# Kernel tuning notes

Hardware: AMD Instinct MI355X
Metric: run time of the kernel (lower is better)

The kernel has to match this reference:

```python
import jax, jax.numpy as jnp
import numpy as np

T = 512        # sequence / max_length
I = 512        # input_dim
H = 1024       # hidden_size
O = 1          # output_size
L = 512        # max_length (attention logits)


def setup_inputs() -> dict:
    key = jax.random.key(0)
    ks = jax.random.split(key, 14)
    s = 0.02
    return {
        "input_seq": jax.random.normal(ks[0], (T, I), jnp.float32),
        "target_seq": jax.random.normal(ks[1], (T, O), jnp.float32),
        # encoder LSTM (input I -> hidden H), PyTorch gate order i,f,g,o
        "W_ih_e": jax.random.normal(ks[2], (4 * H, I), jnp.float32) * s,
        "W_hh_e": jax.random.normal(ks[3], (4 * H, H), jnp.float32) * s,
        "b_ih_e": jnp.zeros((4 * H,), jnp.float32),
        "b_hh_e": jnp.zeros((4 * H,), jnp.float32),
        # attention: Linear(2H -> L)
        "W_attn": jax.random.normal(ks[4], (L, 2 * H), jnp.float32) * s,
        "b_attn": jnp.zeros((L,), jnp.float32),
        # decoder LSTM (input 2H -> hidden H)
        "W_ih_d": jax.random.normal(ks[5], (4 * H, 2 * H), jnp.float32) * s,
        "W_hh_d": jax.random.normal(ks[6], (4 * H, H), jnp.float32) * s,
        "b_ih_d": jnp.zeros((4 * H,), jnp.float32),
        "b_hh_d": jnp.zeros((4 * H,), jnp.float32),
        # output Linear(H -> O)
        "W_out": jax.random.normal(ks[7], (O, H), jnp.float32) * s,
        "b_out": jnp.zeros((O,), jnp.float32),
    }


def _lstm_cell(x, h, c, Wih, Whh, bih, bhh):
    gates = Wih @ x + bih + Whh @ h + bhh          # [4H]
    i, f, g, o = jnp.split(gates, 4)
    c = jax.nn.sigmoid(f) * c + jax.nn.sigmoid(i) * jnp.tanh(g)
    h = jax.nn.sigmoid(o) * jnp.tanh(c)
    return h, c


def reference(input_seq, target_seq, W_ih_e, W_hh_e, b_ih_e, b_hh_e,
              W_attn, b_attn, W_ih_d, W_hh_d, b_ih_d, b_hh_d, W_out, b_out):
    Th = input_seq.shape[0]
    max_len = W_attn.shape[0]
    hid = W_hh_e.shape[1]

    def step(carry, xs):
        eh, ec, dh, dc, aw = carry
        x_t, i = xs
        eh, ec = _lstm_cell(x_t, eh, ec, W_ih_e, W_hh_e, b_ih_e, b_hh_e)
        energy = W_attn @ jnp.concatenate([eh, dh]) + b_attn   # [L]
        aw = aw.at[i].set(energy[i])
        aw = jax.nn.softmax(aw)                                 # re-softmaxed each step, as in source
        context = aw[i] * eh                                    # [H]
        din = jnp.concatenate([context, dh])                    # [2H]
        dh, dc = _lstm_cell(din, dh, dc, W_ih_d, W_hh_d, b_ih_d, b_hh_d)
        out_t = W_out @ dh + b_out                              # [O]
        return (eh, ec, dh, dc, aw), out_t

    z = jnp.zeros((hid,), input_seq.dtype)
    carry0 = (z, z, z, z, jnp.zeros((max_len,), input_seq.dtype))
    _, output_seq = jax.lax.scan(step, carry0, (input_seq, jnp.arange(Th)))
    return output_seq  # [T, O]
```

## Files before the change

kernel.cpp:

```cpp
#include <hip/hip_runtime.h>
#include <math.h>


#define T_STEPS 512
#define ENC_BLK 128
#define NBLK    256
#define SPIN_LIMIT 200000u

typedef float fv4 __attribute__((ext_vector_type(4)));

__device__ __forceinline__ float sigf(float x) { return 1.0f / (1.0f + expf(-x)); }

__device__ __forceinline__ unsigned ld_u(unsigned* p) {
  return __hip_atomic_load(p, __ATOMIC_RELAXED, __HIP_MEMORY_SCOPE_AGENT);
}
__device__ __forceinline__ void st_u(unsigned* p, unsigned v) {
  __hip_atomic_store(p, v, __ATOMIC_RELAXED, __HIP_MEMORY_SCOPE_AGENT);
}

__device__ __forceinline__ fv4 ld_bypass16(const float* p) {
  fv4 v;
  asm volatile("global_load_dwordx4 %0, %1, off sc0 sc1\n\t"
               "s_waitcnt vmcnt(0)"
               : "=&v"(v) : "v"(p) : "memory");
  return v;
}
__device__ __forceinline__ void st_bypass16(float* p, fv4 v) {
  asm volatile("global_store_dwordx4 %0, %1, off sc0 sc1"
               :: "v"(p), "v"(v) : "memory");
}

__device__ __forceinline__ bool valid4(fv4 v) {
  return __float_as_uint(v.x) != 0xAAAAAAAAu && __float_as_uint(v.y) != 0xAAAAAAAAu &&
         __float_as_uint(v.z) != 0xAAAAAAAAu && __float_as_uint(v.w) != 0xAAAAAAAAu;
}

__device__ __forceinline__ fv4 poll_data(const float* p, unsigned* abortf, int* okp) {
  fv4 v;
  unsigned spins = 0;
  int ok = 1;
  for (;;) {
    v = ld_bypass16(p);
    if (valid4(v)) break;
    if (((++spins) & 63u) == 0u) {
      if (ld_u(abortf) != 0u || spins > SPIN_LIMIT) { ok = 0; break; }
    }
  }
  *okp = ok;
  return v;
}

__global__ __launch_bounds__(256) void prep_gemm(const float* __restrict__ X,
                                                 const float* __restrict__ Wih,
                                                 const float* __restrict__ bih,
                                                 const float* __restrict__ bhh,
                                                 float* __restrict__ px,
                                                 unsigned* abortf) {
  if (blockIdx.x == 0 && blockIdx.y == 0 && threadIdx.x == 0) st_u(abortf, 0u);
  __shared__ float Ws[64][68];
  __shared__ float Xs[64][68];
  const int r0 = blockIdx.x * 64;
  const int t0 = blockIdx.y * 64;
  const int tid = threadIdx.x;
  const int tr = tid & 15;
  const int tc = tid >> 4;
  float acc[4][4] = {{0.f}};
  for (int k0 = 0; k0 < 512; k0 += 64) {
    __syncthreads();
    const int lr = tid >> 4;
    const int lc = (tid & 15) * 4;
#pragma unroll
    for (int rep = 0; rep < 4; rep++) {
      const int row = lr + rep * 16;
      const float4 wv = *(const float4*)&Wih[(size_t)(r0 + row) * 512 + k0 + lc];
      Ws[lc + 0][row] = wv.x; Ws[lc + 1][row] = wv.y;
      Ws[lc + 2][row] = wv.z; Ws[lc + 3][row] = wv.w;
      const float4 xv = *(const float4*)&X[(size_t)(t0 + row) * 512 + k0 + lc];
      Xs[row][lc + 0] = xv.x; Xs[row][lc + 1] = xv.y;
      Xs[row][lc + 2] = xv.z; Xs[row][lc + 3] = xv.w;
    }
    __syncthreads();
    for (int kk = 0; kk < 64; kk++) {
      float a[4], x[4];
#pragma unroll
      for (int i = 0; i < 4; i++) a[i] = Ws[kk][tr * 4 + i];
#pragma unroll
      for (int j = 0; j < 4; j++) x[j] = Xs[tc * 4 + j][kk];
#pragma unroll
      for (int i = 0; i < 4; i++)
#pragma unroll
        for (int j = 0; j < 4; j++) acc[i][j] += a[i] * x[j];
    }
  }
#pragma unroll
  for (int i = 0; i < 4; i++) {
    const int r = r0 + tr * 4 + i;
    const int g = r >> 10, h = r & 1023;
    const float bsum = bih[r] + bhh[r];
#pragma unroll
    for (int j = 0; j < 4; j++) {
      const int t = t0 + tc * 4 + j;
      px[((size_t)t * 1024 + h) * 4 + g] = acc[i][j] + bsum;
    }
  }
}

__global__ __launch_bounds__(256, 1) void lstm_persist(
    const float* __restrict__ Whhe, const float* __restrict__ Wattn,
    const float* __restrict__ battn, const float* __restrict__ Wihd,
    const float* __restrict__ Whhd, const float* __restrict__ bihd,
    const float* __restrict__ bhhd, const float* __restrict__ Wout,
    const float* __restrict__ bout, const float* __restrict__ px,
    float* ehbuf, float* dhbuf, unsigned* abortf, float* out) {
  __shared__ float4 xbuf[256];
  __shared__ float4 dbuf[256];
  __shared__ float  aw[512];
  __shared__ float  GA[32];
  __shared__ float  GB[32];
  __shared__ float  redE[4];
  __shared__ float  redE2[4];
  __shared__ float  red[8];
  __shared__ float  red2[4];
  __shared__ float  bd[32];
  __shared__ int    sbad;

  const int b    = blockIdx.x;
  const int tid  = threadIdx.x;
  const int w    = tid >> 6;
  const int lane = tid & 63;
  const int jj   = lane & 7;
  const int seg  = lane >> 3;

  if (b < ENC_BLK) {
    const int e = b;
    const int r = (w << 10) + (e << 3) + jj;
    float4 we[32];
#pragma unroll
    for (int k = 0; k < 32; k++) {
      const int m = (k + seg) & 31;
      we[k] = *(const float4*)&Whhe[(size_t)r * 1024 + seg * 128 + m * 4];
    }
    xbuf[tid] = make_float4(0.f, 0.f, 0.f, 0.f);
    if (tid == 0) sbad = 0;
    float ec = 0.f;
    __syncthreads();

    for (int t = 0; t < T_STEPS; t++) {
      float pxv = 0.f;
      if (seg == 0) pxv = px[((size_t)t * 1024 + (e << 3) + jj) * 4 + w];
      float ge = 0.f;
#pragma unroll
      for (int k = 0; k < 32; k++) {
        const int m = (k + seg) & 31;
        const float4 x = xbuf[seg * 32 + m];
        ge += we[k].x * x.x + we[k].y * x.y + we[k].z * x.z + we[k].w * x.w;
      }
      ge += __shfl_xor(ge, 8, 64);
      ge += __shfl_xor(ge, 16, 64);
      ge += __shfl_xor(ge, 32, 64);
      if (seg == 0) GA[(w << 3) + jj] = ge + pxv;
      __syncthreads();
      float h = 0.f;
      if (tid < 8) {
        const float gi = GA[tid], gf = GA[8 + tid], gg = GA[16 + tid], go = GA[24 + tid];
        const float c = sigf(gf) * ec + sigf(gi) * tanhf(gg);
        ec = c;
        h = sigf(go) * tanhf(c);
      }
      if (w == 0) {
        const int base = lane & 4;
        fv4 pk;
        pk.x = __shfl(h, base + 0, 64); pk.y = __shfl(h, base + 1, 64);
        pk.z = __shfl(h, base + 2, 64); pk.w = __shfl(h, base + 3, 64);
        if (lane == 0 || lane == 4)
          st_bypass16(&ehbuf[(size_t)t * 1024 + (e << 3) + base], pk);
      }
      int ok;
      const fv4 ev = poll_data(&ehbuf[(size_t)t * 1024 + tid * 4], abortf, &ok);
      if (!ok) { st_u(abortf, 1u); sbad = 1; }
      xbuf[tid] = make_float4(ev.x, ev.y, ev.z, ev.w);
      __syncthreads();
      if (sbad) break;
    }
  } else {
    const int d = b - ENC_BLK;
    const int r = (w << 10) + (d << 3) + jj;
    float4 w1[32], wr[32];
#pragma unroll
    for (int k = 0; k < 32; k++) {
      const int m = (k + seg) & 31;
      w1[k] = *(const float4*)&Wihd[(size_t)r * 2048 + seg * 128 + m * 4];
      const float4 a = *(const float4*)&Wihd[(size_t)r * 2048 + 1024 + seg * 128 + m * 4];
      const float4 c = *(const float4*)&Whhd[(size_t)r * 1024 + seg * 128 + m * 4];
      wr[k] = make_float4(a.x + c.x, a.y + c.y, a.z + c.z, a.w + c.w);
    }
    if (tid < 32) {
      const int g = tid >> 3, j = tid & 7;
      bd[tid] = bihd[(g << 10) + (d << 3) + j] + bhhd[(g << 10) + (d << 3) + j];
    }
    xbuf[tid] = make_float4(0.f, 0.f, 0.f, 0.f);
    dbuf[tid] = make_float4(0.f, 0.f, 0.f, 0.f);
    aw[tid] = 0.f; aw[tid + 256] = 0.f;
    if (tid == 0) sbad = 0;
    float dc = 0.f;
    const float4 wo = *(const float4*)&Wout[tid * 4];
    const float boutv = bout[0];
    __syncthreads();

    bool failed = false;
    for (int t = 0; t < T_STEPS; t++) {
      const float4 wae = *(const float4*)&Wattn[(size_t)t * 2048 + tid * 4];
      const float4 wad = *(const float4*)&Wattn[(size_t)t * 2048 + 1024 + tid * 4];
      const float battn_t = battn[t];
      const float ex0 = expf(aw[tid]);
      const float ex1 = expf(aw[tid + 256]);
      float so = ((tid == t) ? 0.f : ex0) + ((tid + 256 == t) ? 0.f : ex1);
#pragma unroll
      for (int mk = 1; mk <= 32; mk <<= 1) so += __shfl_xor(so, mk, 64);
      if (lane == 0) red[w] = so;

      int ok1;
      const fv4 ev = poll_data(&ehbuf[(size_t)t * 1024 + tid * 4], abortf, &ok1);
      if (!ok1) { st_u(abortf, 1u); sbad = 1; }
      float epe = wae.x * ev.x + wae.y * ev.y + wae.z * ev.z + wae.w * ev.w;
#pragma unroll
      for (int mk = 1; mk <= 32; mk <<= 1) epe += __shfl_xor(epe, mk, 64);
      if (lane == 0) redE[w] = epe;
      xbuf[tid] = make_float4(ev.x, ev.y, ev.z, ev.w);
      __syncthreads();
      if (sbad) { failed = true; break; }

      float g1 = 0.f;
#pragma unroll
      for (int k = 0; k < 32; k++) {
        const int m = (k + seg) & 31;
        const float4 x = xbuf[seg * 32 + m];
        g1 += w1[k].x * x.x + w1[k].y * x.y + w1[k].z * x.z + w1[k].w * x.w;
      }
      g1 += __shfl_xor(g1, 8, 64); g1 += __shfl_xor(g1, 16, 64); g1 += __shfl_xor(g1, 32, 64);
      if (seg == 0) GA[(w << 3) + jj] = g1;

      fv4 dv = {0.f, 0.f, 0.f, 0.f};
      float epd = 0.f;
      if (t > 0) {
        int ok2;
        dv = poll_data(&dhbuf[(size_t)(t - 1) * 1024 + tid * 4], abortf, &ok2);
        if (!ok2) { st_u(abortf, 1u); sbad = 1; }
        epd = wad.x * dv.x + wad.y * dv.y + wad.z * dv.z + wad.w * dv.w;
      }
#pragma unroll
      for (int mk = 1; mk <= 32; mk <<= 1) epd += __shfl_xor(epd, mk, 64);
      if (lane == 0) redE2[w] = epd;
      dbuf[tid] = make_float4(dv.x, dv.y, dv.z, dv.w);
      __syncthreads();
      if (sbad) { failed = true; break; }

      float g2 = 0.f;
#pragma unroll
      for (int k = 0; k < 32; k++) {
        const int m = (k + seg) & 31;
        const float4 dd = dbuf[seg * 32 + m];
        g2 += wr[k].x * dd.x + wr[k].y * dd.y + wr[k].z * dd.z + wr[k].w * dd.w;
      }
      g2 += __shfl_xor(g2, 8, 64); g2 += __shfl_xor(g2, 16, 64); g2 += __shfl_xor(g2, 32, 64);
      if (seg == 0) GB[(w << 3) + jj] = g2;

      const float sum_other = red[0] + red[1] + red[2] + red[3];
      const float e_t = redE[0] + redE[1] + redE[2] + redE[3] +
                        redE2[0] + redE2[1] + redE2[2] + redE2[3] + battn_t;
      const float exden = expf(e_t);
      const float inv = 1.f / (sum_other + exden);
      aw[tid] = ((tid == t) ? exden : ex0) * inv;
      aw[tid + 256] = ((tid + 256 == t) ? exden : ex1) * inv;
      const float awt = exden * inv;
      __syncthreads();

      float h = 0.f;
      if (tid < 8) {
        const float gi = awt * GA[tid]      + GB[tid]      + bd[tid];
        const float gf = awt * GA[8 + tid]  + GB[8 + tid]  + bd[8 + tid];
        const float gg = awt * GA[16 + tid] + GB[16 + tid] + bd[16 + tid];
        const float go = awt * GA[24 + tid] + GB[24 + tid] + bd[24 + tid];
        const float c = sigf(gf) * dc + sigf(gi) * tanhf(gg);
        dc = c;
        h = sigf(go) * tanhf(c);
      }
      if (w == 0) {
        const int base = lane & 4;
        fv4 pk;
        pk.x = __shfl(h, base + 0, 64); pk.y = __shfl(h, base + 1, 64);
        pk.z = __shfl(h, base + 2, 64); pk.w = __shfl(h, base + 3, 64);
        if (lane == 0 || lane == 4)
          st_bypass16(&dhbuf[(size_t)t * 1024 + (d << 3) + base], pk);
      }
    }

    if (!failed) {
#pragma unroll
      for (int i = 0; i < 4; i++) {
        const int t = d * 4 + i;
        int ok;
        const fv4 dv = poll_data(&dhbuf[(size_t)t * 1024 + tid * 4], abortf, &ok);
        if (!ok) break;
        float op = wo.x * dv.x + wo.y * dv.y + wo.z * dv.z + wo.w * dv.w;
#pragma unroll
        for (int mk = 1; mk <= 32; mk <<= 1) op += __shfl_xor(op, mk, 64);
        if (lane == 0) red2[w] = op;
        __syncthreads();
        if (tid == 0) out[t] = red2[0] + red2[1] + red2[2] + red2[3] + boutv;
        __syncthreads();
      }
    }
  }
}

extern "C" void kernel_launch(void* const* d_in, const int* in_sizes, int n_in,
                              void* d_out, int out_size, void* d_ws, size_t ws_size,
                              hipStream_t stream) {
  const float* X     = (const float*)d_in[0];
  const float* Wihe  = (const float*)d_in[2];
  const float* Whhe  = (const float*)d_in[3];
  const float* bihe  = (const float*)d_in[4];
  const float* bhhe  = (const float*)d_in[5];
  const float* Wattn = (const float*)d_in[6];
  const float* battn = (const float*)d_in[7];
  const float* Wihd  = (const float*)d_in[8];
  const float* Whhd  = (const float*)d_in[9];
  const float* bihd  = (const float*)d_in[10];
  const float* bhhd  = (const float*)d_in[11];
  const float* Wo    = (const float*)d_in[12];
  const float* bo    = (const float*)d_in[13];
  float* out = (float*)d_out;

  float* ws    = (float*)d_ws;
  float* px    = ws;
  float* ehbuf = px + (size_t)T_STEPS * 1024 * 4;
  float* dhbuf = ehbuf + (size_t)T_STEPS * 1024;
  unsigned* abortf = (unsigned*)(dhbuf + (size_t)T_STEPS * 1024);
  const size_t need = ((size_t)T_STEPS * 1024 * 6) * sizeof(float) + sizeof(unsigned);
  if (ws_size < need) return;

  prep_gemm<<<dim3(64, 8), 256, 0, stream>>>(X, Wihe, bihe, bhhe, px, abortf);
  lstm_persist<<<NBLK, 256, 0, stream>>>(
      Whhe, Wattn, battn, Wihd, Whhd, bihd, bhhd, Wo, bo, px, ehbuf, dhbuf,
      abortf, out);
}
```

Before: 2.087 ms.

## Replicate hidden-state exchange buffers to spread polling traffic and add backoff

Each producer now writes its hidden-state values into up to eight replicas of the eh/dh exchange buffers, and each block polls the replica chosen by its block index. This is meant to cut contention from 256 blocks spinning on the same cache lines. The polling loop also gains s_sleep backoff after a few failed tries, and the packed 16-byte stores become per-lane 4-byte stores. The cost is more store traffic, more workspace, and possibly slower reaction to newly published data because of the sleep.

After: 2.114 ms. Within noise of the previous version (+1.3%).

```diff
diff --git a/kernel.cpp b/kernel.cpp
--- a/kernel.cpp
+++ b/kernel.cpp
@@ -6,6 +6,7 @@
 #define ENC_BLK 128
 #define NBLK    256
 #define SPIN_LIMIT 200000u
+#define REP_STRIDE ((size_t)T_STEPS * 1024)
 
 typedef float fv4 __attribute__((ext_vector_type(4)));
 
@@ -25,8 +26,8 @@
                : "=&v"(v) : "v"(p) : "memory");
   return v;
 }
-__device__ __forceinline__ void st_bypass16(float* p, fv4 v) {
-  asm volatile("global_store_dwordx4 %0, %1, off sc0 sc1"
+__device__ __forceinline__ void st_bypass4(float* p, float v) {
+  asm volatile("global_store_dword %0, %1, off sc0 sc1"
                :: "v"(p), "v"(v) : "memory");
 }
 
@@ -42,7 +43,9 @@
   for (;;) {
     v = ld_bypass16(p);
     if (valid4(v)) break;
-    if (((++spins) & 63u) == 0u) {
+    ++spins;
+    if (spins > 4u) __builtin_amdgcn_s_sleep(1);
+    if ((spins & 63u) == 0u) {
       if (ld_u(abortf) != 0u || spins > SPIN_LIMIT) { ok = 0; break; }
     }
   }
@@ -111,7 +114,7 @@
     const float* __restrict__ Whhd, const float* __restrict__ bihd,
     const float* __restrict__ bhhd, const float* __restrict__ Wout,
     const float* __restrict__ bout, const float* __restrict__ px,
-    float* ehbuf, float* dhbuf, unsigned* abortf, float* out) {
+    float* ehbuf, float* dhbuf, int nrep, unsigned* abortf, float* out) {
   __shared__ float4 xbuf[256];
   __shared__ float4 dbuf[256];
   __shared__ float  aw[512];
@@ -130,6 +133,7 @@
   const int lane = tid & 63;
   const int jj   = lane & 7;
   const int seg  = lane >> 3;
+  const size_t myrep = (size_t)(b & (nrep - 1)) * REP_STRIDE;
 
   if (b < ENC_BLK) {
     const int e = b;
@@ -160,23 +164,16 @@
       ge += __shfl_xor(ge, 32, 64);
       if (seg == 0) GA[(w << 3) + jj] = ge + pxv;
       __syncthreads();
-      float h = 0.f;
       if (tid < 8) {
         const float gi = GA[tid], gf = GA[8 + tid], gg = GA[16 + tid], go = GA[24 + tid];
         const float c = sigf(gf) * ec + sigf(gi) * tanhf(gg);
         ec = c;
-        h = sigf(go) * tanhf(c);
-      }
-      if (w == 0) {
-        const int base = lane & 4;
-        fv4 pk;
-        pk.x = __shfl(h, base + 0, 64); pk.y = __shfl(h, base + 1, 64);
-        pk.z = __shfl(h, base + 2, 64); pk.w = __shfl(h, base + 3, 64);
-        if (lane == 0 || lane == 4)
-          st_bypass16(&ehbuf[(size_t)t * 1024 + (e << 3) + base], pk);
+        const float h = sigf(go) * tanhf(c);
+        for (int rp = 0; rp < nrep; rp++)
+          st_bypass4(&ehbuf[(size_t)rp * REP_STRIDE + (size_t)t * 1024 + (e << 3) + tid], h);
       }
       int ok;
-      const fv4 ev = poll_data(&ehbuf[(size_t)t * 1024 + tid * 4], abortf, &ok);
+      const fv4 ev = poll_data(&ehbuf[myrep + (size_t)t * 1024 + tid * 4], abortf, &ok);
       if (!ok) { st_u(abortf, 1u); sbad = 1; }
       xbuf[tid] = make_float4(ev.x, ev.y, ev.z, ev.w);
       __syncthreads();
@@ -220,7 +217,7 @@
       if (lane == 0) red[w] = so;
 
       int ok1;
-      const fv4 ev = poll_data(&ehbuf[(size_t)t * 1024 + tid * 4], abortf, &ok1);
+      const fv4 ev = poll_data(&ehbuf[myrep + (size_t)t * 1024 + tid * 4], abortf, &ok1);
       if (!ok1) { st_u(abortf, 1u); sbad = 1; }
       float epe = wae.x * ev.x + wae.y * ev.y + wae.z * ev.z + wae.w * ev.w;
 #pragma unroll
@@ -244,7 +241,7 @@
       float epd = 0.f;
       if (t > 0) {
         int ok2;
-        dv = poll_data(&dhbuf[(size_t)(t - 1) * 1024 + tid * 4], abortf, &ok2);
+        dv = poll_data(&dhbuf[myrep + (size_t)(t - 1) * 1024 + tid * 4], abortf, &ok2);
         if (!ok2) { st_u(abortf, 1u); sbad = 1; }
         epd = wad.x * dv.x + wad.y * dv.y + wad.z * dv.z + wad.w * dv.w;
       }
@@ -275,7 +272,6 @@
       const float awt = exden * inv;
       __syncthreads();
 
-      float h = 0.f;
       if (tid < 8) {
         const float gi = awt * GA[tid]      + GB[tid]      + bd[tid];
         const float gf = awt * GA[8 + tid]  + GB[8 + tid]  + bd[8 + tid];
@@ -283,15 +279,9 @@
         const float go = awt * GA[24 + tid] + GB[24 + tid] + bd[24 + tid];
         const float c = sigf(gf) * dc + sigf(gi) * tanhf(gg);
         dc = c;
-        h = sigf(go) * tanhf(c);
-      }
-      if (w == 0) {
-        const int base = lane & 4;
-        fv4 pk;
-        pk.x = __shfl(h, base + 0, 64); pk.y = __shfl(h, base + 1, 64);
-        pk.z = __shfl(h, base + 2, 64); pk.w = __shfl(h, base + 3, 64);
-        if (lane == 0 || lane == 4)
-          st_bypass16(&dhbuf[(size_t)t * 1024 + (d << 3) + base], pk);
+        const float h = sigf(go) * tanhf(c);
+        for (int rp = 0; rp < nrep; rp++)
+          st_bypass4(&dhbuf[(size_t)rp * REP_STRIDE + (size_t)t * 1024 + (d << 3) + tid], h);
       }
     }
 
@@ -300,7 +290,7 @@
       for (int i = 0; i < 4; i++) {
         const int t = d * 4 + i;
         int ok;
-        const fv4 dv = poll_data(&dhbuf[(size_t)t * 1024 + tid * 4], abortf, &ok);
+        const fv4 dv = poll_data(&dhbuf[myrep + (size_t)t * 1024 + tid * 4], abortf, &ok);
         if (!ok) break;
         float op = wo.x * dv.x + wo.y * dv.y + wo.z * dv.z + wo.w * dv.w;
 #pragma unroll
@@ -332,16 +322,23 @@
   const float* bo    = (const float*)d_in[13];
   float* out = (float*)d_out;
 
+  const size_t px_elems = (size_t)T_STEPS * 1024 * 4;
+  int nrep = 8;
+  size_t need;
+  for (;; nrep >>= 1) {
+    need = (px_elems + 2 * (size_t)nrep * REP_STRIDE) * sizeof(float) + sizeof(unsigned);
+    if (need <= ws_size || nrep == 1) break;
+  }
+  if (ws_size < need) return;
+
   float* ws    = (float*)d_ws;
   float* px    = ws;
-  float* ehbuf = px + (size_t)T_STEPS * 1024 * 4;
-  float* dhbuf = ehbuf + (size_t)T_STEPS * 1024;
-  unsigned* abortf = (unsigned*)(dhbuf + (size_t)T_STEPS * 1024);
-  const size_t need = ((size_t)T_STEPS * 1024 * 6) * sizeof(float) + sizeof(unsigned);
-  if (ws_size < need) return;
+  float* ehbuf = px + px_elems;
+  float* dhbuf = ehbuf + (size_t)nrep * REP_STRIDE;
+  unsigned* abortf = (unsigned*)(dhbuf + (size_t)nrep * REP_STRIDE);
 
   prep_gemm<<<dim3(64, 8), 256, 0, stream>>>(X, Wihe, bihe, bhhe, px, abortf);
   lstm_persist<<<NBLK, 256, 0, stream>>>(
       Whhe, Wattn, battn, Wihd, Whhd, bihd, bhhd, Wo, bo, px, ehbuf, dhbuf,
-      abortf, out);
-}
+      nrep, abortf, out);
+}
```
